# Kernel optimization log

Hardware: AMD Instinct MI355X
Metric: run time of the kernel (lower is better)

The kernel has to match this reference:

```python
import jax, jax.numpy as jnp
import numpy as np


def setup_inputs() -> dict:
    key = jax.random.key(0)
    k1, k2, k3, k4, k5, k6 = jax.random.split(key, 6)
    B, N, K = 2, 60000, 16
    C_in, C_add, C_mid = 64, 3, 16
    out_features = 128
    in_features = (C_in + C_add) * C_mid  # 1072
    return {
        "input_features": jax.random.normal(k1, (B, N, C_in), dtype=jnp.float32),
        "neighbor_inds": jax.random.randint(k2, (B, N, K), 0, N, dtype=jnp.int32),
        "weightnet": jax.random.normal(k3, (B, N, K, C_mid), dtype=jnp.float32),
        "additional_features": jax.random.normal(k4, (B, N, K, C_add), dtype=jnp.float32),
        "linear_weight": jax.random.normal(k5, (out_features, in_features), dtype=jnp.float32) * 0.03,
        "linear_bias": jax.random.normal(k6, (out_features,), dtype=jnp.float32),
    }


def reference(input_features, neighbor_inds, weightnet, additional_features, linear_weight, linear_bias):
    # Gather neighbor features: [B, N, K, C_in]
    gathered = jax.vmap(lambda feats, idx: feats[idx])(input_features, neighbor_inds)
    # Concat per-neighbor additional features: [B, N, K, C_in + C_add]
    feat = jnp.concatenate([gathered, additional_features], axis=-1)
    # PConv: contract over neighbors K against weightnet -> [B, N, C, M]
    pconv = jnp.einsum('bnkc,bnkm->bncm', feat, weightnet)
    B, N = pconv.shape[0], pconv.shape[1]
    pconv = pconv.reshape(B, N, -1)  # [B, N, (C_in+C_add)*C_mid]
    # Fused linear projection
    return jnp.einsum('bnf,of->bno', pconv, linear_weight) + linear_bias
```

## Files before the change

kernel.cpp:

```cpp
#include <hip/hip_runtime.h>

#define NPTS  60000
#define NBLK  3750
#define FP    1088
#define PSTR  1096

typedef _Float16 f16x4 __attribute__((ext_vector_type(4)));
typedef _Float16 f16x8 __attribute__((ext_vector_type(8)));
typedef float    f32x4 __attribute__((ext_vector_type(4)));

__global__ void __launch_bounds__(256)
cvt_lw_kernel(const float* __restrict__ LW, _Float16* __restrict__ LWh) {
    const int o = blockIdx.x;
    for (int f = threadIdx.x; f < FP; f += 256) {
        const float v = (f < 1072) ? LW[o * 1072 + f] : 0.f;
        LWh[(f >> 5) * (128 * 32) + o * 32 + (f & 31)] = (_Float16)v;
    }
}

struct GRegs {
    float fv[4][4];
    float wv[4];
    float av[4];
};

static __device__ __forceinline__ void issue_gather(
    const float* __restrict__ inF, const float* __restrict__ Wn,
    const float* __restrict__ addF, int bbase, int base_nk,
    int ind_lane, int i, int q, int ml, bool mlo, GRegs& g)
{
    #pragma unroll
    for (int j = 0; j < 4; ++j) {
        const int k   = q * 4 + j;
        const int idx = __shfl(ind_lane, i * 16 + k, 64);
        const float* fp = inF + (bbase + idx) * 64 + ml;
        #pragma unroll
        for (int ct = 0; ct < 4; ++ct)
            g.fv[ct][j] = fp[ct * 16];
        g.wv[j] = Wn[(base_nk + k) * 16 + ml];
        g.av[j] = mlo ? addF[(base_nk + k) * 3 + ml] : 0.f;
    }
}

static __device__ __forceinline__ void compute_point(
    const GRegs& g, _Float16* sProw, int qsw, int ml, bool mlo)
{
    const f32x4 z4 = {0.f, 0.f, 0.f, 0.f};
    f16x4 aW, bA;
    #pragma unroll
    for (int j = 0; j < 4; ++j) { aW[j] = (_Float16)g.wv[j]; bA[j] = (_Float16)g.av[j]; }

    #pragma unroll
    for (int ct = 0; ct < 4; ++ct) {
        f16x4 bF;
        #pragma unroll
        for (int j = 0; j < 4; ++j) bF[j] = (_Float16)g.fv[ct][j];
        const f32x4 d = __builtin_amdgcn_mfma_f32_16x16x16f16(aW, bF, z4, 0, 0, 0);
        f16x4 dh;
        #pragma unroll
        for (int r = 0; r < 4; ++r) dh[r] = (_Float16)d[r];
        *(f16x4*)&sProw[(ct * 16 + ml) * 16 + qsw * 4] = dh;
    }
    const f32x4 d = __builtin_amdgcn_mfma_f32_16x16x16f16(aW, bA, z4, 0, 0, 0);
    if (mlo) {
        f16x4 dh;
        #pragma unroll
        for (int r = 0; r < 4; ++r) dh[r] = (_Float16)d[r];
        *(f16x4*)&sProw[(64 + ml) * 16 + qsw * 4] = dh;
    }
}

__global__ void __launch_bounds__(512, 8)
pconv_linear_mfma(const float* __restrict__ inF,
                  const int*   __restrict__ inds,
                  const float* __restrict__ Wn,
                  const float* __restrict__ addF,
                  const _Float16* __restrict__ LWh,
                  const float* __restrict__ bias,
                  float*       __restrict__ out)
{
    __shared__ __align__(16) _Float16 sP[16 * PSTR];

    const int t    = threadIdx.x;
    const int lane = t & 63;
    const int w    = t >> 6;
    const int q    = lane >> 4;
    const int ml   = lane & 15;
    const bool mlo = (ml < 3);
    const int qsw  = q ^ (((ml >> 2) & 1) << 1);

    const int bid   = blockIdx.x;
    const int b     = bid / NBLK;
    const int n0    = (bid - b * NBLK) * 16;
    const int bbase = b * NPTS;

    const int ind_lane = inds[(bbase + n0 + w * 2) * 16 + (lane & 31)];

    if (t < 256)
        sP[(t >> 4) * PSTR + 1072 + (t & 15)] = (_Float16)0.f;

    const int nk0 = (bbase + n0 + w * 2) * 16;
    _Float16* sPw = sP + (w * 2) * PSTR;
    GRegs g0, g1;
    issue_gather(inF, Wn, addF, bbase, nk0,      ind_lane, 0, q, ml, mlo, g0);
    issue_gather(inF, Wn, addF, bbase, nk0 + 16, ind_lane, 1, q, ml, mlo, g1);
    compute_point(g0, sPw,        qsw, ml, mlo);
    compute_point(g1, sPw + PSTR, qsw, ml, mlo);
    __syncthreads();

    const int o0 = w * 16;
    const float bz = bias[o0 + ml];
    f32x4 acc = {0.f, 0.f, 0.f, 0.f};
    const _Float16* aP = sP + ml * PSTR + (q >> 1) * 16 + (q & 1) * 8;
    const int flip = (q & 1) ? -8 : 8;
    const _Float16* bP = LWh + (o0 + ml) * 32 + q * 8;

    #pragma unroll 4
    for (int ch = 0; ch < 34; ++ch) {
        const int off = ch * 32 + ((ch & 2) ? flip : 0);
        f16x8 a = *(const f16x8*)(aP + off);
        f16x8 b = *(const f16x8*)(bP + ch * 4096);
        acc = __builtin_amdgcn_mfma_f32_16x16x32_f16(a, b, acc, 0, 0, 0);
    }

    float* obase = out + (bbase + n0 + q * 4) * 128 + o0 + ml;
    #pragma unroll
    for (int r = 0; r < 4; ++r)
        obase[r * 128] = acc[r] + bz;
}

extern "C" void kernel_launch(void* const* d_in, const int* in_sizes, int n_in,
                              void* d_out, int out_size, void* d_ws, size_t ws_size,
                              hipStream_t stream)
{
    const float* inF  = (const float*)d_in[0];
    const int*   inds = (const int*)  d_in[1];
    const float* Wn   = (const float*)d_in[2];
    const float* addF = (const float*)d_in[3];
    const float* LW   = (const float*)d_in[4];
    const float* bias = (const float*)d_in[5];
    float* out = (float*)d_out;
    _Float16* LWh = (_Float16*)d_ws;

    cvt_lw_kernel<<<dim3(128), dim3(256), 0, stream>>>(LW, LWh);
    pconv_linear_mfma<<<dim3(2 * NBLK), dim3(512), 0, stream>>>(
        inF, inds, Wn, addF, LWh, bias, out);
}
```

Measured before the change: 374.9 us.

## Process 32 points per block to reuse linear weights across two MFMA tiles

Each block now handles 32 points instead of 16. Every wave gathers four points, interleaving the next gathers with the current compute, and the linear stage reuses each loaded weight fragment for two accumulator tiles. The aim is to halve the global reads of the fp16 linear weights per point and to overlap gather latency with compute. In exchange, shared memory per block doubles (about 70KB, now dynamic) and the occupancy hint drops from 8 to 4, which reduces the number of waves available to hide memory latency.

After: 346.2 us. 7.7% less time.

```diff
diff --git a/kernel.cpp b/kernel.cpp
--- a/kernel.cpp
+++ b/kernel.cpp
@@ -1,9 +1,10 @@
 #include <hip/hip_runtime.h>
 
 #define NPTS  60000
-#define NBLK  3750
+#define NBLK  1875
 #define FP    1088
 #define PSTR  1096
+#define SPBYTES (32 * PSTR * 2)
 
 typedef _Float16 f16x4 __attribute__((ext_vector_type(4)));
 typedef _Float16 f16x8 __attribute__((ext_vector_type(8)));
@@ -70,7 +71,7 @@
     }
 }
 
-__global__ void __launch_bounds__(512, 8)
+__global__ void __launch_bounds__(512, 4)
 pconv_linear_mfma(const float* __restrict__ inF,
                   const int*   __restrict__ inds,
                   const float* __restrict__ Wn,
@@ -79,7 +80,7 @@
                   const float* __restrict__ bias,
                   float*       __restrict__ out)
 {
-    __shared__ __align__(16) _Float16 sP[16 * PSTR];
+    extern __shared__ __align__(16) _Float16 sP[];
 
     const int t    = threadIdx.x;
     const int lane = t & 63;
@@ -91,42 +92,53 @@
 
     const int bid   = blockIdx.x;
     const int b     = bid / NBLK;
-    const int n0    = (bid - b * NBLK) * 16;
+    const int n0    = (bid - b * NBLK) * 32;
     const int bbase = b * NPTS;
 
-    const int ind_lane = inds[(bbase + n0 + w * 2) * 16 + (lane & 31)];
+    const int ind_lane = inds[(bbase + n0 + w * 4) * 16 + lane];
 
-    if (t < 256)
-        sP[(t >> 4) * PSTR + 1072 + (t & 15)] = (_Float16)0.f;
+    sP[(t >> 4) * PSTR + 1072 + (t & 15)] = (_Float16)0.f;
 
-    const int nk0 = (bbase + n0 + w * 2) * 16;
-    _Float16* sPw = sP + (w * 2) * PSTR;
+    const int nk0 = (bbase + n0 + w * 4) * 16;
+    _Float16* sPw = sP + (w * 4) * PSTR;
     GRegs g0, g1;
     issue_gather(inF, Wn, addF, bbase, nk0,      ind_lane, 0, q, ml, mlo, g0);
     issue_gather(inF, Wn, addF, bbase, nk0 + 16, ind_lane, 1, q, ml, mlo, g1);
-    compute_point(g0, sPw,        qsw, ml, mlo);
-    compute_point(g1, sPw + PSTR, qsw, ml, mlo);
+    compute_point(g0, sPw,            qsw, ml, mlo);
+    issue_gather(inF, Wn, addF, bbase, nk0 + 32, ind_lane, 2, q, ml, mlo, g0);
+    compute_point(g1, sPw + PSTR,     qsw, ml, mlo);
+    issue_gather(inF, Wn, addF, bbase, nk0 + 48, ind_lane, 3, q, ml, mlo, g1);
+    compute_point(g0, sPw + 2 * PSTR, qsw, ml, mlo);
+    compute_point(g1, sPw + 3 * PSTR, qsw, ml, mlo);
     __syncthreads();
 
     const int o0 = w * 16;
     const float bz = bias[o0 + ml];
-    f32x4 acc = {0.f, 0.f, 0.f, 0.f};
-    const _Float16* aP = sP + ml * PSTR + (q >> 1) * 16 + (q & 1) * 8;
+    f32x4 acc0 = {0.f, 0.f, 0.f, 0.f};
+    f32x4 acc1 = {0.f, 0.f, 0.f, 0.f};
+    const _Float16* aP0 = sP + ml * PSTR + (q >> 1) * 16 + (q & 1) * 8;
+    const _Float16* aP1 = aP0 + 16 * PSTR;
     const int flip = (q & 1) ? -8 : 8;
     const _Float16* bP = LWh + (o0 + ml) * 32 + q * 8;
 
-    #pragma unroll 4
+    #pragma unroll 2
     for (int ch = 0; ch < 34; ++ch) {
         const int off = ch * 32 + ((ch & 2) ? flip : 0);
-        f16x8 a = *(const f16x8*)(aP + off);
-        f16x8 b = *(const f16x8*)(bP + ch * 4096);
-        acc = __builtin_amdgcn_mfma_f32_16x16x32_f16(a, b, acc, 0, 0, 0);
+        f16x8 bf = *(const f16x8*)(bP + ch * 4096);
+        f16x8 a0 = *(const f16x8*)(aP0 + off);
+        f16x8 a1 = *(const f16x8*)(aP1 + off);
+        acc0 = __builtin_amdgcn_mfma_f32_16x16x32_f16(a0, bf, acc0, 0, 0, 0);
+        acc1 = __builtin_amdgcn_mfma_f32_16x16x32_f16(a1, bf, acc1, 0, 0, 0);
     }
 
-    float* obase = out + (bbase + n0 + q * 4) * 128 + o0 + ml;
+    float* ob = out + (bbase + n0 + q * 4) * 128 + o0 + ml;
     #pragma unroll
     for (int r = 0; r < 4; ++r)
-        obase[r * 128] = acc[r] + bz;
+        ob[r * 128] = acc0[r] + bz;
+    ob += 16 * 128;
+    #pragma unroll
+    for (int r = 0; r < 4; ++r)
+        ob[r * 128] = acc1[r] + bz;
 }
 
 extern "C" void kernel_launch(void* const* d_in, const int* in_sizes, int n_in,
@@ -142,7 +154,10 @@
     float* out = (float*)d_out;
     _Float16* LWh = (_Float16*)d_ws;
 
+    hipFuncSetAttribute((const void*)pconv_linear_mfma,
+                        hipFuncAttributeMaxDynamicSharedMemorySize, SPBYTES);
+
     cvt_lw_kernel<<<dim3(128), dim3(256), 0, stream>>>(LW, LWh);
-    pconv_linear_mfma<<<dim3(2 * NBLK), dim3(512), 0, stream>>>(
+    pconv_linear_mfma<<<dim3(2 * NBLK), dim3(512), SPBYTES, stream>>>(
         inF, inds, Wn, addF, LWh, bias, out);
 }
```
